# Kernel tuning notes

Hardware: AMD Instinct MI355X
Metric: run time of the kernel (lower is better)

Reference implementation:

```python
import jax, jax.numpy as jnp
import numpy as np


def rgb2hsv(rgb):
    # skimage-style rgb2hsv, all channels in [0,1]
    r, g, b = rgb[..., 0], rgb[..., 1], rgb[..., 2]
    maxc = jnp.max(rgb, axis=-1)
    minc = jnp.min(rgb, axis=-1)
    delta = maxc - minc
    safe_d = jnp.where(delta == 0, 1.0, delta)
    h = jnp.where(maxc == r, (g - b) / safe_d,
        jnp.where(maxc == g, 2.0 + (b - r) / safe_d,
                             4.0 + (r - g) / safe_d))
    h = (h / 6.0) % 1.0
    h = jnp.where(delta == 0, 0.0, h)
    safe_m = jnp.where(maxc == 0, 1.0, maxc)
    s = jnp.where(maxc == 0, 0.0, delta / safe_m)
    return jnp.stack([h, s, maxc], axis=-1)


def setup_inputs() -> dict:
    key = jax.random.key(0)
    ks = jax.random.split(key, 5)
    N = 4194304
    gt = jax.random.uniform(ks[0], (N, 3), dtype=jnp.float32)
    BG_map = jax.random.uniform(ks[1], (N, 3), dtype=jnp.float32)
    FG_map = jax.random.uniform(ks[2], (N, 3), dtype=jnp.float32)
    FG_acc = jax.random.uniform(ks[3], (N,), dtype=jnp.float32)
    # positive uncertainties (beta), avoid zeros
    FG_uncertainties = jax.random.uniform(ks[4], (N, 1), dtype=jnp.float32) + 0.1
    threshold_param = jnp.float32(-2.0)
    steepness = jnp.float32(0.1)
    return {"gt": gt, "BG_map": BG_map, "FG_map": FG_map, "FG_acc": FG_acc,
            "FG_uncertainties": FG_uncertainties,
            "threshold_param": threshold_param, "steepness": steepness,
            "iter": 1000}


def reference(gt, BG_map, FG_map, FG_acc, FG_uncertainties,
              threshold_param, steepness, iter):
    threshold = 1.414 * (1.0 - jax.nn.sigmoid(threshold_param))
    # Original round-trips through CPU numpy (no grad, BG_map detached):
    gt_hsv = rgb2hsv(jax.lax.stop_gradient(gt))
    bg_hsv = rgb2hsv(jax.lax.stop_gradient(BG_map))
    dhv = gt_hsv[..., (0, 2)] - bg_hsv[..., (0, 2)]  # [N,2] (H and V channels)
    diff = jnp.linalg.norm(dhv, axis=-1)             # [N]
    mask = jax.nn.sigmoid((diff - threshold) / 0.1)  # [N]
    if iter > 300:
        BG_loss = jnp.mean((gt - BG_map) ** 2, axis=-1) * (1.0 - mask)  # [N]
        u = FG_uncertainties[..., 0]  # [N]
        FG_perray = jnp.mean((gt - FG_map) ** 2, axis=-1) / (2.0 * u * u) + jnp.log(u)
        FG_loss = FG_perray * mask
        return jnp.mean(BG_loss, axis=-1) + jnp.mean(FG_loss, axis=-1)
    else:
        return jnp.mean((gt - BG_map) ** 2)
```

## Files before the change

kernel.cpp:

```cpp
#include <hip/hip_runtime.h>
#include <math.h>

#define THREADS 256
#define PPT 4

__device__ __forceinline__ float frcp(float x)  { return __builtin_amdgcn_rcpf(x); }
__device__ __forceinline__ float fsqrt(float x) { return __builtin_amdgcn_sqrtf(x); }

__device__ __forceinline__ float fast_sigmoid(float x) {
    return frcp(1.0f + __expf(-x));
}

__device__ __forceinline__ void rgb2hv(float r, float g, float b,
                                       float& h, float& v) {
    float maxc = fmaxf(r, fmaxf(g, b));
    float minc = fminf(r, fminf(g, b));
    float delta = maxc - minc;
    float rd = frcp((delta == 0.0f) ? 1.0f : delta);
    float hh;
    if (maxc == r)      hh = (g - b) * rd;
    else if (maxc == g) hh = 2.0f + (b - r) * rd;
    else                hh = 4.0f + (r - g) * rd;
    hh = hh * (1.0f / 6.0f);
    hh = hh - floorf(hh);
    h = (delta == 0.0f) ? 0.0f : hh;
    v = maxc;
}

__device__ __forceinline__ float pixel_loss(
    float gr, float gg, float gb,
    float br, float bgc, float bb,
    float fr, float fgc, float fb,
    float u, float threshold, int it)
{
    if (it > 300) {
        float hg, vg, hb, vb;
        rgb2hv(gr, gg, gb, hg, vg);
        rgb2hv(br, bgc, bb, hb, vb);
        float dh = hg - hb;
        float dv = vg - vb;
        float diff = fsqrt(dh * dh + dv * dv);
        float mask = fast_sigmoid((diff - threshold) * 10.0f);

        float d0 = gr - br, d1 = gg - bgc, d2 = gb - bb;
        float bg_mse = (d0 * d0 + d1 * d1 + d2 * d2) * (1.0f / 3.0f);

        float e0 = gr - fr, e1 = gg - fgc, e2 = gb - fb;
        float fg_mse = (e0 * e0 + e1 * e1 + e2 * e2) * (1.0f / 3.0f);
        float fg_perray = fg_mse * 0.5f * frcp(u * u) + __logf(u);

        return bg_mse + (fg_perray - bg_mse) * mask;
    } else {
        float d0 = gr - br, d1 = gg - bgc, d2 = gb - bb;
        return d0 * d0 + d1 * d1 + d2 * d2;
    }
}

__global__ __launch_bounds__(THREADS) void loss_kernel(
    const float* __restrict__ gt, const float* __restrict__ bg,
    const float* __restrict__ fg, const float* __restrict__ unc,
    const float* __restrict__ thr_param, const int* __restrict__ iter_p,
    double* __restrict__ partials, int n_pix)
{
    const int t = blockIdx.x * blockDim.x + threadIdx.x;
    const int p0 = t * PPT;
    const int it = iter_p[0];
    const float threshold = 1.414f * (1.0f - fast_sigmoid(thr_param[0]));

    float local = 0.0f;

    if (p0 + PPT <= n_pix) {
        const float4* g4 = (const float4*)gt + 3 * t;
        const float4* b4 = (const float4*)bg + 3 * t;
        const float4* f4 = (const float4*)fg + 3 * t;
        float4 ga = g4[0], gbv = g4[1], gc = g4[2];
        float4 ba = b4[0], bbv = b4[1], bc = b4[2];
        float4 fa = f4[0], fbv = f4[1], fc = f4[2];
        float4 u4 = *(const float4*)(unc + p0);

        float G[12] = {ga.x, ga.y, ga.z, ga.w, gbv.x, gbv.y, gbv.z, gbv.w,
                       gc.x, gc.y, gc.z, gc.w};
        float B[12] = {ba.x, ba.y, ba.z, ba.w, bbv.x, bbv.y, bbv.z, bbv.w,
                       bc.x, bc.y, bc.z, bc.w};
        float F[12] = {fa.x, fa.y, fa.z, fa.w, fbv.x, fbv.y, fbv.z, fbv.w,
                       fc.x, fc.y, fc.z, fc.w};
        float U[4] = {u4.x, u4.y, u4.z, u4.w};

        #pragma unroll
        for (int j = 0; j < PPT; ++j) {
            local += pixel_loss(G[3*j], G[3*j+1], G[3*j+2],
                                B[3*j], B[3*j+1], B[3*j+2],
                                F[3*j], F[3*j+1], F[3*j+2],
                                U[j], threshold, it);
        }
    } else if (p0 < n_pix) {
        for (int p = p0; p < n_pix; ++p) {
            local += pixel_loss(gt[3*p], gt[3*p+1], gt[3*p+2],
                                bg[3*p], bg[3*p+1], bg[3*p+2],
                                fg[3*p], fg[3*p+1], fg[3*p+2],
                                unc[p], threshold, it);
        }
    }

    #pragma unroll
    for (int off = 32; off > 0; off >>= 1)
        local += __shfl_down(local, off, 64);

    __shared__ double wsum[THREADS / 64];
    const int lane = threadIdx.x & 63;
    const int wid = threadIdx.x >> 6;
    if (lane == 0) wsum[wid] = (double)local;
    __syncthreads();
    if (threadIdx.x == 0) {
        double s = 0.0;
        #pragma unroll
        for (int w = 0; w < THREADS / 64; ++w) s += wsum[w];
        partials[blockIdx.x] = s;
    }
}

__global__ void loss_kernel_atomic_init(double* accum) { *accum = 0.0; }

__global__ __launch_bounds__(1024) void finalize_kernel(
    const double* __restrict__ partials, int n_part,
    const int* __restrict__ iter_p, float* __restrict__ out, int n_pix)
{
    double s = 0.0;
    for (int i = threadIdx.x; i < n_part; i += 1024)
        s += partials[i];
    #pragma unroll
    for (int off = 32; off > 0; off >>= 1)
        s += __shfl_down(s, off, 64);

    __shared__ double wsum[16];
    const int lane = threadIdx.x & 63;
    const int wid = threadIdx.x >> 6;
    if (lane == 0) wsum[wid] = s;
    __syncthreads();
    if (threadIdx.x == 0) {
        double tot = 0.0;
        #pragma unroll
        for (int w = 0; w < 16; ++w) tot += wsum[w];
        double denom = (iter_p[0] > 300) ? (double)n_pix : 3.0 * (double)n_pix;
        out[0] = (float)(tot / denom);
    }
}

extern "C" void kernel_launch(void* const* d_in, const int* in_sizes, int n_in,
                              void* d_out, int out_size, void* d_ws, size_t ws_size,
                              hipStream_t stream) {
    const float* gt  = (const float*)d_in[0];
    const float* bg  = (const float*)d_in[1];
    const float* fg  = (const float*)d_in[2];
    const float* unc = (const float*)d_in[4];
    const float* thr = (const float*)d_in[5];
    const int*  iter = (const int*)d_in[7];

    const int n_pix = in_sizes[0] / 3;
    const int total_threads = (n_pix + PPT - 1) / PPT;
    const int blocks = (total_threads + THREADS - 1) / THREADS;

    double* partials = (double*)d_ws;

    if ((size_t)blocks * sizeof(double) <= ws_size) {
        loss_kernel<<<blocks, THREADS, 0, stream>>>(gt, bg, fg, unc, thr, iter,
                                                    partials, n_pix);
        finalize_kernel<<<1, 1024, 0, stream>>>(partials, blocks, iter,
                                                (float*)d_out, n_pix);
    } else {
        loss_kernel_atomic_init<<<1, 1, 0, stream>>>(partials);
        loss_kernel<<<blocks, THREADS, 0, stream>>>(gt, bg, fg, unc, thr, iter,
                                                    partials, n_pix);
        finalize_kernel<<<1, 1024, 0, stream>>>(partials, 1, iter,
                                                (float*)d_out, n_pix);
    }
}
```

Measured before the change: 33.43 us.

## Stage pixel chunks into LDS with async global_load_lds double buffering

Each block now handles 2048 pixels in four chunks of 512. Every chunk of gt/bg/fg is copied into a double-buffered LDS area with global_load_lds, so the next chunk is fetched while the current one is computed. Threads then read pixels from LDS with a stride of 3 floats, and leftover pixels go to a separate tail kernel. This adds LDS traffic, a __syncthreads per chunk and 36 KB of LDS per block, which may lower occupancy. There is also no explicit wait on the async loads before they are read.

```diff
diff --git a/kernel.cpp b/kernel.cpp
--- a/kernel.cpp
+++ b/kernel.cpp
@@ -1,15 +1,31 @@
 #include <hip/hip_runtime.h>
 #include <math.h>
-
-#define THREADS 256
-#define PPT 4
+#include <stdint.h>
+
+#define THREADS   256
+#define CHUNK_PX  512
+#define CHUNKS    4
+#define BLOCK_PX  (CHUNK_PX * CHUNKS)
+#define SEG_B     (CHUNK_PX * 12)
+#define BUF_B     (3 * SEG_B)
+#define GROUPS    (BUF_B / 16 / 64)
 
 __device__ __forceinline__ float frcp(float x)  { return __builtin_amdgcn_rcpf(x); }
 __device__ __forceinline__ float fsqrt(float x) { return __builtin_amdgcn_sqrtf(x); }
-
 __device__ __forceinline__ float fast_sigmoid(float x) {
     return frcp(1.0f + __expf(-x));
 }
+
+#if __has_builtin(__builtin_amdgcn_global_load_lds)
+#define GLDS16(gsrc, ldst)                                                  \
+    __builtin_amdgcn_global_load_lds(                                       \
+        (const __attribute__((address_space(1))) uint32_t*)(gsrc),          \
+        (__attribute__((address_space(3))) uint32_t*)(ldst), 16, 0, 0)
+#else
+#define GLDS16(gsrc, ldst)                                                  \
+    do { *(float4*)((char*)(ldst) + (threadIdx.x & 63) * 16) =              \
+         *(const float4*)(gsrc); } while (0)
+#endif
 
 __device__ __forceinline__ void rgb2hv(float r, float g, float b,
                                        float& h, float& v) {
@@ -56,50 +72,73 @@
     }
 }
 
+__device__ __forceinline__ void stage_chunk(
+    const float4* __restrict__ g4, const float4* __restrict__ b4,
+    const float4* __restrict__ f4, char* buf, int pix0)
+{
+    const int wave = threadIdx.x >> 6;
+    const int lane = threadIdx.x & 63;
+    const int gbase = (pix0 * 3) >> 2;
+    #pragma unroll
+    for (int k = 0; k < 5; ++k) {
+        const int g = k * 4 + wave;
+        if (g < GROUPS) {
+            const int u = g * 64;
+            const float4* src;
+            if (u < 384)      src = g4 + (gbase + u + lane);
+            else if (u < 768) src = b4 + (gbase + (u - 384) + lane);
+            else              src = f4 + (gbase + (u - 768) + lane);
+            GLDS16(src, buf + u * 16);
+        }
+    }
+}
+
+__device__ __forceinline__ float compute_chunk(
+    const char* buf, const float* __restrict__ unc, int pix0,
+    float threshold, int it)
+{
+    const float* gB = (const float*)buf;
+    const float* bB = (const float*)(buf + SEG_B);
+    const float* fB = (const float*)(buf + 2 * SEG_B);
+    float acc = 0.0f;
+    #pragma unroll
+    for (int k = 0; k < CHUNK_PX / THREADS; ++k) {
+        const int l = threadIdx.x + k * THREADS;
+        const float u = unc[pix0 + l];
+        acc += pixel_loss(gB[3*l], gB[3*l+1], gB[3*l+2],
+                          bB[3*l], bB[3*l+1], bB[3*l+2],
+                          fB[3*l], fB[3*l+1], fB[3*l+2],
+                          u, threshold, it);
+    }
+    return acc;
+}
+
 __global__ __launch_bounds__(THREADS) void loss_kernel(
     const float* __restrict__ gt, const float* __restrict__ bg,
     const float* __restrict__ fg, const float* __restrict__ unc,
     const float* __restrict__ thr_param, const int* __restrict__ iter_p,
-    double* __restrict__ partials, int n_pix)
-{
-    const int t = blockIdx.x * blockDim.x + threadIdx.x;
-    const int p0 = t * PPT;
+    double* __restrict__ partials)
+{
+    __shared__ char lds[2][BUF_B];
     const int it = iter_p[0];
     const float threshold = 1.414f * (1.0f - fast_sigmoid(thr_param[0]));
+    const int block_pix0 = blockIdx.x * BLOCK_PX;
+
+    const float4* g4 = (const float4*)gt;
+    const float4* b4 = (const float4*)bg;
+    const float4* f4 = (const float4*)fg;
+
+    stage_chunk(g4, b4, f4, lds[0], block_pix0);
 
     float local = 0.0f;
-
-    if (p0 + PPT <= n_pix) {
-        const float4* g4 = (const float4*)gt + 3 * t;
-        const float4* b4 = (const float4*)bg + 3 * t;
-        const float4* f4 = (const float4*)fg + 3 * t;
-        float4 ga = g4[0], gbv = g4[1], gc = g4[2];
-        float4 ba = b4[0], bbv = b4[1], bc = b4[2];
-        float4 fa = f4[0], fbv = f4[1], fc = f4[2];
-        float4 u4 = *(const float4*)(unc + p0);
-
-        float G[12] = {ga.x, ga.y, ga.z, ga.w, gbv.x, gbv.y, gbv.z, gbv.w,
-                       gc.x, gc.y, gc.z, gc.w};
-        float B[12] = {ba.x, ba.y, ba.z, ba.w, bbv.x, bbv.y, bbv.z, bbv.w,
-                       bc.x, bc.y, bc.z, bc.w};
-        float F[12] = {fa.x, fa.y, fa.z, fa.w, fbv.x, fbv.y, fbv.z, fbv.w,
-                       fc.x, fc.y, fc.z, fc.w};
-        float U[4] = {u4.x, u4.y, u4.z, u4.w};
-
-        #pragma unroll
-        for (int j = 0; j < PPT; ++j) {
-            local += pixel_loss(G[3*j], G[3*j+1], G[3*j+2],
-                                B[3*j], B[3*j+1], B[3*j+2],
-                                F[3*j], F[3*j+1], F[3*j+2],
-                                U[j], threshold, it);
-        }
-    } else if (p0 < n_pix) {
-        for (int p = p0; p < n_pix; ++p) {
-            local += pixel_loss(gt[3*p], gt[3*p+1], gt[3*p+2],
-                                bg[3*p], bg[3*p+1], bg[3*p+2],
-                                fg[3*p], fg[3*p+1], fg[3*p+2],
-                                unc[p], threshold, it);
-        }
+    #pragma unroll
+    for (int c = 0; c < CHUNKS; ++c) {
+        __syncthreads();
+        if (c + 1 < CHUNKS)
+            stage_chunk(g4, b4, f4, lds[(c + 1) & 1],
+                        block_pix0 + (c + 1) * CHUNK_PX);
+        local += compute_chunk(lds[c & 1], unc, block_pix0 + c * CHUNK_PX,
+                               threshold, it);
     }
 
     #pragma unroll
@@ -119,7 +158,35 @@
     }
 }
 
-__global__ void loss_kernel_atomic_init(double* accum) { *accum = 0.0; }
+__global__ __launch_bounds__(THREADS) void tail_kernel(
+    const float* __restrict__ gt, const float* __restrict__ bg,
+    const float* __restrict__ fg, const float* __restrict__ unc,
+    const float* __restrict__ thr_param, const int* __restrict__ iter_p,
+    double* __restrict__ partials, int start, int end, int slot)
+{
+    const int it = iter_p[0];
+    const float threshold = 1.414f * (1.0f - fast_sigmoid(thr_param[0]));
+    float local = 0.0f;
+    for (int p = start + (int)threadIdx.x; p < end; p += THREADS)
+        local += pixel_loss(gt[3*p], gt[3*p+1], gt[3*p+2],
+                            bg[3*p], bg[3*p+1], bg[3*p+2],
+                            fg[3*p], fg[3*p+1], fg[3*p+2],
+                            unc[p], threshold, it);
+    #pragma unroll
+    for (int off = 32; off > 0; off >>= 1)
+        local += __shfl_down(local, off, 64);
+    __shared__ double wsum[THREADS / 64];
+    const int lane = threadIdx.x & 63;
+    const int wid = threadIdx.x >> 6;
+    if (lane == 0) wsum[wid] = (double)local;
+    __syncthreads();
+    if (threadIdx.x == 0) {
+        double s = 0.0;
+        #pragma unroll
+        for (int w = 0; w < THREADS / 64; ++w) s += wsum[w];
+        partials[slot] = s;
+    }
+}
 
 __global__ __launch_bounds__(1024) void finalize_kernel(
     const double* __restrict__ partials, int n_part,
@@ -131,7 +198,6 @@
     #pragma unroll
     for (int off = 32; off > 0; off >>= 1)
         s += __shfl_down(s, off, 64);
-
     __shared__ double wsum[16];
     const int lane = threadIdx.x & 63;
     const int wid = threadIdx.x >> 6;
@@ -157,21 +223,28 @@
     const int*  iter = (const int*)d_in[7];
 
     const int n_pix = in_sizes[0] / 3;
-    const int total_threads = (n_pix + PPT - 1) / PPT;
-    const int blocks = (total_threads + THREADS - 1) / THREADS;
+    int blocks = n_pix / BLOCK_PX;
+    const int rem_start = blocks * BLOCK_PX;
+    const int rem = n_pix - rem_start;
+    int n_part = blocks + (rem > 0 ? 1 : 0);
 
     double* partials = (double*)d_ws;
 
-    if ((size_t)blocks * sizeof(double) <= ws_size) {
-        loss_kernel<<<blocks, THREADS, 0, stream>>>(gt, bg, fg, unc, thr, iter,
-                                                    partials, n_pix);
-        finalize_kernel<<<1, 1024, 0, stream>>>(partials, blocks, iter,
-                                                (float*)d_out, n_pix);
-    } else {
-        loss_kernel_atomic_init<<<1, 1, 0, stream>>>(partials);
-        loss_kernel<<<blocks, THREADS, 0, stream>>>(gt, bg, fg, unc, thr, iter,
-                                                    partials, n_pix);
+    if ((size_t)n_part * sizeof(double) > ws_size) {
+        tail_kernel<<<1, THREADS, 0, stream>>>(gt, bg, fg, unc, thr, iter,
+                                               partials, 0, n_pix, 0);
         finalize_kernel<<<1, 1024, 0, stream>>>(partials, 1, iter,
                                                 (float*)d_out, n_pix);
-    }
-}
+        return;
+    }
+
+    if (blocks > 0)
+        loss_kernel<<<blocks, THREADS, 0, stream>>>(gt, bg, fg, unc, thr, iter,
+                                                    partials);
+    if (rem > 0)
+        tail_kernel<<<1, THREADS, 0, stream>>>(gt, bg, fg, unc, thr, iter,
+                                               partials, rem_start, n_pix,
+                                               blocks);
+    finalize_kernel<<<1, 1024, 0, stream>>>(partials, n_part, iter,
+                                            (float*)d_out, n_pix);
+}
```

Result: slower. 34.78 us (+4.0%).
